# Performance work log

Hardware: AMD Instinct MI355X
Metric: run time of the kernel (lower is better)

Reference implementation:

```python
import math
import jax, jax.numpy as jnp
import numpy as np

D_MODEL = 1024
N_HEADS = 16
HEAD_DIM = D_MODEL // N_HEADS
B, L = 1, 4096


def _slopes(n_heads):
    ratio = 2.0 ** (-8.0 / n_heads)
    return jnp.asarray([ratio ** (i + 1) for i in range(n_heads)], dtype=jnp.float32)


def setup_inputs() -> dict:
    key = jax.random.key(0)
    ks = jax.random.split(key, 5)
    scale = 1.0 / math.sqrt(D_MODEL)
    return {
        "x": jax.random.normal(ks[0], (B, L, D_MODEL), dtype=jnp.float32),
        "q_w": jax.random.normal(ks[1], (D_MODEL, D_MODEL), dtype=jnp.float32) * scale,
        "k_w": jax.random.normal(ks[2], (D_MODEL, D_MODEL), dtype=jnp.float32) * scale,
        "v_w": jax.random.normal(ks[3], (D_MODEL, D_MODEL), dtype=jnp.float32) * scale,
        "o_w": jax.random.normal(ks[4], (D_MODEL, D_MODEL), dtype=jnp.float32) * scale,
    }


def reference(x, q_w, k_w, v_w, o_w):
    b, l, _ = x.shape
    # projections -> [B, H, L, hd]
    def proj(w):
        return (x @ w).reshape(b, l, N_HEADS, HEAD_DIM).transpose(0, 2, 1, 3)
    q, k, v = proj(q_w), proj(k_w), proj(v_w)

    scale = math.sqrt(HEAD_DIM)
    scores = jnp.einsum("bhid,bhjd->bhij", q, k) / scale  # [B,H,L,L]

    pos = jnp.arange(l)
    distance = jnp.abs(pos[None, :] - pos[:, None]).astype(jnp.float32)  # [L,L]
    alibi = -distance[None, :, :] * _slopes(N_HEADS)[:, None, None]       # [H,L,L]
    scores = scores + alibi[None]

    causal = pos[None, :] <= pos[:, None]  # j <= i
    scores = jnp.where(causal[None, None], scores, -jnp.inf)

    attn = jax.nn.softmax(scores, axis=-1)
    out = jnp.einsum("bhij,bhjd->bhid", attn, v)
    out = out.transpose(0, 2, 1, 3).reshape(b, l, D_MODEL)
    return out @ o_w
```

## Files before the change

kernel.cpp:

```cpp
#include <hip/hip_runtime.h>

#define L_SEQ 4096
#define DM    1024
#define NH    16
#define HD    64

typedef unsigned short ushort_t;
typedef __attribute__((ext_vector_type(8))) short bf16x8;
typedef __attribute__((ext_vector_type(4))) float f32x4;

__device__ inline unsigned short f2bf(float f) {
    union { float f; unsigned int u; } v; v.f = f;
    unsigned int r = v.u + 0x7fffu + ((v.u >> 16) & 1u);
    return (unsigned short)(r >> 16);
}

__device__ inline unsigned cvt_pk_bf16(float lo, float hi) {
    unsigned w;
    asm("v_cvt_pk_bf16_f32 %0, %1, %2" : "=v"(w) : "v"(lo), "v"(hi));
    return w;
}

__device__ inline void load_lds16(const ushort_t* g, ushort_t* l) {
    __builtin_amdgcn_global_load_lds(
        (const __attribute__((address_space(1))) unsigned int*)g,
        (__attribute__((address_space(3))) unsigned int*)l, 16, 0, 0);
}

__device__ inline bool detect_f32(const ushort_t* xraw) {
    __shared__ int s_flag;
    const int t = threadIdx.x;
    if (t < 64) {
        unsigned e = (xraw[2 * t] >> 7) & 0xFFu;
        unsigned long long m = __ballot(e >= 0x88u);
        if (t == 0) s_flag = (__popcll(m) >= 8) ? 1 : 0;
    }
    __syncthreads();
    return s_flag != 0;
}

__global__ __launch_bounds__(256) void convert_all(const void* __restrict__ xv,
                                                   const void* __restrict__ w0,
                                                   const void* __restrict__ w1,
                                                   const void* __restrict__ w2,
                                                   const void* __restrict__ w3,
                                                   ushort_t* __restrict__ xb,
                                                   ushort_t* __restrict__ wT) {
    bool f32 = detect_f32((const ushort_t*)xv);
    const int z = blockIdx.z;
    const int t = threadIdx.x;

    if (z == 4) {
        const int B0 = (blockIdx.y * 16 + blockIdx.x) * 16384;
        #pragma unroll
        for (int it = 0; it < 8; ++it) {
            const int i = B0 + it * 2048 + t * 8;
            if (f32) {
                const float* xf = (const float*)xv;
                float4 v0 = *(const float4*)(xf + i);
                float4 v1 = *(const float4*)(xf + i + 4);
                uint4 u;
                u.x = cvt_pk_bf16(v0.x, v0.y);
                u.y = cvt_pk_bf16(v0.z, v0.w);
                u.z = cvt_pk_bf16(v1.x, v1.y);
                u.w = cvt_pk_bf16(v1.z, v1.w);
                *(uint4*)(xb + i) = u;
            } else {
                *(uint4*)(xb + i) = *(const uint4*)((const ushort_t*)xv + i);
            }
        }
        return;
    }

    const void* w = (z == 0) ? w0 : (z == 1) ? w1 : (z == 2) ? w2 : w3;
    ushort_t* out = wT + (size_t)z * (DM * DM);
    __shared__ ushort_t T[64][65];
    const int k0 = blockIdx.x * 64, n0 = blockIdx.y * 64;
    #pragma unroll
    for (int i = 0; i < 16; ++i) {
        int e = t + i * 256;
        int r = e >> 6, c = e & 63;
        T[r][c] = f32 ? f2bf(((const float*)w)[(size_t)(k0 + r) * DM + n0 + c])
                      : ((const ushort_t*)w)[(size_t)(k0 + r) * DM + n0 + c];
    }
    __syncthreads();
    #pragma unroll
    for (int i = 0; i < 16; ++i) {
        int e = t + i * 256;
        int d = e >> 6, l = e & 63;
        out[(size_t)(n0 + d) * DM + k0 + l] = T[l][d];
    }
}

__device__ inline void gemm128_body(const ushort_t* __restrict__ A,
                                    const ushort_t* __restrict__ Bt,
                                    void* __restrict__ Cv, int cmode,
                                    int m0, int n0) {
    constexpr int K = 1024, NOUT = 1024;
    __shared__ ushort_t As[128 * 64];
    __shared__ ushort_t Bs[128 * 64];

    const int t = threadIdx.x, lane = t & 63, wave = t >> 6;
    const int l15 = lane & 15, quad = lane >> 4;
    const int mw = (wave >> 1) * 64, nw = (wave & 1) * 64;
    const int srow = lane >> 3;
    const int sgr  = (lane & 7) ^ (lane >> 3);
    const int swz  = l15 & 7;

    f32x4 acc[4][4] = {};

    for (int k0 = 0; k0 < K; k0 += 64) {
        #pragma unroll
        for (int i = 0; i < 4; ++i) {
            const int j = wave * 4 + i;
            load_lds16(A  + (size_t)(m0 + 8 * j + srow) * K + k0 + sgr * 8,
                       &As[8 * j * 64]);
            load_lds16(Bt + (size_t)(n0 + 8 * j + srow) * K + k0 + sgr * 8,
                       &Bs[8 * j * 64]);
        }
        __syncthreads();

        #pragma unroll
        for (int kt = 0; kt < 2; ++kt) {
            bf16x8 af[4], bf[4];
            #pragma unroll
            for (int i = 0; i < 4; ++i) {
                af[i] = *(const bf16x8*)&As[(mw + i * 16 + l15) * 64
                                            + (((kt * 4 + quad) ^ swz) * 8)];
                bf[i] = *(const bf16x8*)&Bs[(nw + i * 16 + l15) * 64
                                            + (((kt * 4 + quad) ^ swz) * 8)];
            }
            #pragma unroll
            for (int mt = 0; mt < 4; ++mt)
                #pragma unroll
                for (int nt = 0; nt < 4; ++nt)
                    acc[mt][nt] = __builtin_amdgcn_mfma_f32_16x16x32_bf16(
                        af[mt], bf[nt], acc[mt][nt], 0, 0, 0);
        }
        __syncthreads();
    }

    if (cmode == 2) {
        ushort_t* Vt = (ushort_t*)Cv;
        #pragma unroll
        for (int mt = 0; mt < 4; ++mt)
            #pragma unroll
            for (int nt = 0; nt < 4; ++nt) {
                int col  = n0 + nw + nt * 16 + l15;
                int row0 = m0 + mw + mt * 16 + quad * 4;
                ushort_t pk[4] = {f2bf(acc[mt][nt][0]), f2bf(acc[mt][nt][1]),
                                  f2bf(acc[mt][nt][2]), f2bf(acc[mt][nt][3])};
                *(uint2*)&Vt[(size_t)col * L_SEQ + row0] = *(const uint2*)pk;
            }
        return;
    }

    const int odd = lane & 1;
    #pragma unroll
    for (int mtp = 0; mtp < 2; ++mtp)
        #pragma unroll
        for (int nt = 0; nt < 4; ++nt)
            #pragma unroll
            for (int r = 0; r < 4; ++r) {
                float zA = acc[2 * mtp][nt][r];
                float zB = acc[2 * mtp + 1][nt][r];
                float send = odd ? zA : zB;
                float got  = __shfl_xor(send, 1);
                const int row = m0 + mw + (2 * mtp + odd) * 16 + quad * 4 + r;
                const int col = n0 + nw + nt * 16 + (l15 & ~1);
                if (cmode == 1) {
                    float2 w2 = odd ? make_float2(got, zB) : make_float2(zA, got);
                    *(float2*)((float*)Cv + (size_t)row * NOUT + col) = w2;
                } else {
                    float lo = odd ? got : zA;
                    float hi = odd ? zB  : got;
                    unsigned w = cvt_pk_bf16(lo, hi);
                    *(unsigned*)((ushort_t*)Cv + (size_t)row * NOUT + col) = w;
                }
            }
}

__global__ __launch_bounds__(256) void qkv128(const ushort_t* __restrict__ xb,
                                              const ushort_t* __restrict__ wT,
                                              ushort_t* Qp, ushort_t* Kp, ushort_t* Vt) {
    const int b = blockIdx.x;
    const int n0 = (b & 7) * 128;
    const int u  = b >> 3;
    const int m0 = (u / 3) * 128;
    const int z  = u % 3;
    const ushort_t* Bt = wT + (size_t)z * (DM * DM);
    if (z == 0)      gemm128_body(xb, Bt, Qp, 0, m0, n0);
    else if (z == 1) gemm128_body(xb, Bt, Kp, 0, m0, n0);
    else             gemm128_body(xb, Bt, Vt, 2, m0, n0);
}

__global__ __launch_bounds__(256) void ogemm128(const void* __restrict__ xdet,
                                                const ushort_t* __restrict__ An,
                                                const ushort_t* __restrict__ woT,
                                                void* __restrict__ C) {
    bool f32 = detect_f32((const ushort_t*)xdet);
    const int b = blockIdx.x;
    const int n0 = (b & 7) * 128, m0 = (b >> 3) * 128;
    gemm128_body(An, woT, C, f32 ? 1 : 0, m0, n0);
}

__global__ __launch_bounds__(256) void attn_kernel(const ushort_t* __restrict__ Q,
                                                   const ushort_t* __restrict__ Kp,
                                                   const ushort_t* __restrict__ Vt,
                                                   ushort_t* __restrict__ O) {
    __shared__ ushort_t Ks[2][128 * 64];
    __shared__ ushort_t Vs[2][64 * 128];
    __shared__ ushort_t Pt[64 * 128];

    const int b    = blockIdx.x;
    const int h    = 2 * (b & 7) + ((b >> 3) & 1);
    const int bx   = b >> 4;
    const int t    = threadIdx.x;
    const int lane = t & 63, wave = t >> 6;
    const int l15  = lane & 15, quad = lane >> 4;
    const float LOG2E  = 1.44269504f;
    const float slope2 = exp2f(-0.5f * (float)(h + 1)) * LOG2E;
    const float c0     = 0.125f * LOG2E;
    const float qd4f   = (float)(quad * 4);

    const int krow = lane >> 3, kgr = (lane & 7) ^ (lane >> 3);
    const int vsub = lane >> 4;
    const int swz = l15 & 7;

    auto stage_load = [&](int buf, int kv0) {
        #pragma unroll
        for (int i = 0; i < 4; ++i) {
            const int j = wave * 4 + i;
            const int r = 8 * j + krow;
            load_lds16(Kp + (size_t)(kv0 + r) * DM + h * HD + kgr * 8,
                       &Ks[buf][8 * j * 64]);
        }
        #pragma unroll
        for (int i = 0; i < 4; ++i) {
            const int j = wave * 4 + i;
            const int d = 4 * j + vsub;
            const int g = (lane & 15) ^ (4 * (j & 1) + vsub);
            load_lds16(Vt + (size_t)(h * HD + d) * L_SEQ + kv0 + g * 8,
                       &Vs[buf][4 * j * 128]);
        }
    };

    int par = 0;
    stage_load(0, 0);

    #pragma unroll
    for (int half = 0; half < 2; ++half) {
        const int qb = half ? bx : (63 - bx);
        const int q0 = qb * 64;
        const int qg = q0 + wave * 16 + l15;
        const float qf = (float)qg;

        bf16x8 bq[2];
        #pragma unroll
        for (int kt = 0; kt < 2; ++kt)
            bq[kt] = *(const bf16x8*)(Q + (size_t)qg * DM + h * HD + kt * 32 + quad * 8);

        f32x4 acc_o[4] = {};
        float l_r = 0.f;

        const int nst = (qb + 2) >> 1;
        for (int s = 0; s < nst; ++s) {
            const int kv0 = s * 128;
            __syncthreads();

            const int nkv0 = (s + 1 < nst) ? (s + 1) * 128 : 0;
            stage_load(par ^ 1, nkv0);

            f32x4 sacc[8];
            #pragma unroll
            for (int mt = 0; mt < 8; ++mt) sacc[mt] = (f32x4){0.f, 0.f, 0.f, 0.f};
            #pragma unroll
            for (int kt = 0; kt < 2; ++kt)
                #pragma unroll
                for (int mt = 0; mt < 8; ++mt) {
                    bf16x8 a = *(const bf16x8*)&Ks[par][(mt * 16 + l15) * 64
                                                        + (((kt * 4 + quad) ^ swz) * 8)];
                    sacc[mt] = __builtin_amdgcn_mfma_f32_16x16x32_bf16(a, bq[kt], sacc[mt], 0, 0, 0);
                }

            const bool diag = (kv0 + 128 > q0);
            const float off = slope2 * ((float)kv0 + qd4f - qf);
            float rs = 0.f;
            #pragma unroll
            for (int mt = 0; mt < 8; ++mt)
                #pragma unroll
                for (int r = 0; r < 4; ++r) {
                    float kvl = (float)(mt * 16 + r);
                    float s2  = fmaf(sacc[mt][r], c0, fmaf(slope2, kvl, off));
                    if (diag) {
                        int kvg = kv0 + mt * 16 + quad * 4 + r;
                        s2 = (kvg <= qg) ? s2 : -1e30f;
                    }
                    float p = exp2f(s2);
                    sacc[mt][r] = p;
                    rs += p;
                }
            rs += __shfl_xor(rs, 16);
            rs += __shfl_xor(rs, 32);
            l_r += rs;

            #pragma unroll
            for (int mt = 0; mt < 8; ++mt) {
                union { float f; unsigned u; } a0, a1, a2, a3;
                a0.f = sacc[mt][0]; a1.f = sacc[mt][1];
                a2.f = sacc[mt][2]; a3.f = sacc[mt][3];
                uint2 w;
                w.x = __builtin_amdgcn_perm(a1.u, a0.u, 0x07060302);
                w.y = __builtin_amdgcn_perm(a3.u, a2.u, 0x07060302);
                const int g = mt * 2 + (quad >> 1);
                *(uint2*)&Pt[(wave * 16 + l15) * 128
                             + ((g ^ swz) * 8 + (quad & 1) * 4)] = w;
            }
            __threadfence_block();

            #pragma unroll
            for (int kt = 0; kt < 4; ++kt) {
                bf16x8 a = *(const bf16x8*)&Pt[(wave * 16 + l15) * 128
                                               + (((kt * 4 + quad) ^ swz) * 8)];
                #pragma unroll
                for (int nt = 0; nt < 4; ++nt) {
                    bf16x8 bvv = *(const bf16x8*)&Vs[par][(nt * 16 + l15) * 128
                                                          + (((kt * 4 + quad) ^ swz) * 8)];
                    acc_o[nt] = __builtin_amdgcn_mfma_f32_16x16x32_bf16(a, bvv, acc_o[nt], 0, 0, 0);
                }
            }

            par ^= 1;
        }

        float linv[4];
        #pragma unroll
        for (int r = 0; r < 4; ++r) linv[r] = 1.0f / __shfl(l_r, quad * 4 + r);
        #pragma unroll
        for (int nt = 0; nt < 4; ++nt)
            #pragma unroll
            for (int r = 0; r < 4; ++r) {
                int row = q0 + wave * 16 + quad * 4 + r;
                O[(size_t)row * DM + h * HD + nt * 16 + l15] = f2bf(acc_o[nt][r] * linv[r]);
            }
    }
}

extern "C" void kernel_launch(void* const* d_in, const int* in_sizes, int n_in,
                              void* d_out, int out_size, void* d_ws, size_t ws_size,
                              hipStream_t stream) {
    const void* x  = d_in[0];
    const void* wq = d_in[1];
    const void* wk = d_in[2];
    const void* wv = d_in[3];
    const void* wo = d_in[4];

    const size_t SZ = (size_t)L_SEQ * DM;
    const size_t WZ = (size_t)DM * DM;
    ushort_t* xb = (ushort_t*)d_ws;
    ushort_t* wT = xb + SZ;
    ushort_t* Qp = wT + 4 * WZ;
    ushort_t* Kp = Qp + SZ;
    ushort_t* Vt = Kp + SZ;
    ushort_t* An = xb;

    convert_all<<<dim3(16, 16, 5), 256, 0, stream>>>(x, wq, wk, wv, wo, xb, wT);
    qkv128<<<768, 256, 0, stream>>>(xb, wT, Qp, Kp, Vt);
    attn_kernel<<<512, 256, 0, stream>>>(Qp, Kp, Vt, An);
    ogemm128<<<256, 256, 0, stream>>>(x, An, wT + 3 * WZ, d_out);
}
```

Measured before the change: 243.7 us.

## Fuse paired causal query blocks into one KV sweep sharing K/V tiles

Each attention block previously processed its two paired query blocks (63-bx and bx) in sequence, loading every K/V tile twice for the overlapping prefix. Now both query blocks run in a single loop over KV tiles. Each staged K/V tile is reused for block B while B is still in range. Block index order is also remapped so pairings alternate in workload across the grid. This roughly halves K/V LDS staging traffic and barriers for the short block. The cost is more registers for the two accumulator sets and score arrays, which may lower occupancy.

```diff
diff --git a/kernel.cpp b/kernel.cpp
--- a/kernel.cpp
+++ b/kernel.cpp
@@ -214,7 +214,8 @@
 
     const int b    = blockIdx.x;
     const int h    = 2 * (b & 7) + ((b >> 3) & 1);
-    const int bx   = b >> 4;
+    const int pi   = b >> 4;
+    const int bx   = (pi < 16) ? pi : (47 - pi);
     const int t    = threadIdx.x;
     const int lane = t & 63, wave = t >> 6;
     const int l15  = lane & 15, quad = lane >> 4;
@@ -245,70 +246,135 @@
         }
     };
 
+    const int qbA = 63 - bx, qbB = bx;
+    const int q0A = qbA * 64, q0B = qbB * 64;
+    const int qgA = q0A + wave * 16 + l15;
+    const int qgB = q0B + wave * 16 + l15;
+    const float qfA = (float)qgA, qfB = (float)qgB;
+    const int nstA = (qbA + 2) >> 1;
+    const int nstB = (qbB + 2) >> 1;
+
+    bf16x8 bqA[2], bqB[2];
+    #pragma unroll
+    for (int kt = 0; kt < 2; ++kt) {
+        bqA[kt] = *(const bf16x8*)(Q + (size_t)qgA * DM + h * HD + kt * 32 + quad * 8);
+        bqB[kt] = *(const bf16x8*)(Q + (size_t)qgB * DM + h * HD + kt * 32 + quad * 8);
+    }
+
+    f32x4 accA[4] = {}, accB[4] = {};
+    float lA = 0.f, lB = 0.f;
+
     int par = 0;
     stage_load(0, 0);
 
-    #pragma unroll
-    for (int half = 0; half < 2; ++half) {
-        const int qb = half ? bx : (63 - bx);
-        const int q0 = qb * 64;
-        const int qg = q0 + wave * 16 + l15;
-        const float qf = (float)qg;
-
-        bf16x8 bq[2];
+    for (int s = 0; s < nstA; ++s) {
+        const int kv0 = s * 128;
+        const bool doB = (s < nstB);
+        __syncthreads();
+
+        const int nkv0 = (s + 1 < nstA) ? (s + 1) * 128 : 0;
+        stage_load(par ^ 1, nkv0);
+
+        f32x4 sA[8], sB[8];
+        #pragma unroll
+        for (int mt = 0; mt < 8; ++mt) sA[mt] = (f32x4){0.f, 0.f, 0.f, 0.f};
         #pragma unroll
         for (int kt = 0; kt < 2; ++kt)
-            bq[kt] = *(const bf16x8*)(Q + (size_t)qg * DM + h * HD + kt * 32 + quad * 8);
-
-        f32x4 acc_o[4] = {};
-        float l_r = 0.f;
-
-        const int nst = (qb + 2) >> 1;
-        for (int s = 0; s < nst; ++s) {
-            const int kv0 = s * 128;
-            __syncthreads();
-
-            const int nkv0 = (s + 1 < nst) ? (s + 1) * 128 : 0;
-            stage_load(par ^ 1, nkv0);
-
-            f32x4 sacc[8];
-            #pragma unroll
-            for (int mt = 0; mt < 8; ++mt) sacc[mt] = (f32x4){0.f, 0.f, 0.f, 0.f};
+            #pragma unroll
+            for (int mt = 0; mt < 8; ++mt) {
+                bf16x8 a = *(const bf16x8*)&Ks[par][(mt * 16 + l15) * 64
+                                                    + (((kt * 4 + quad) ^ swz) * 8)];
+                sA[mt] = __builtin_amdgcn_mfma_f32_16x16x32_bf16(a, bqA[kt], sA[mt], 0, 0, 0);
+            }
+        if (doB) {
+            #pragma unroll
+            for (int mt = 0; mt < 8; ++mt) sB[mt] = (f32x4){0.f, 0.f, 0.f, 0.f};
             #pragma unroll
             for (int kt = 0; kt < 2; ++kt)
                 #pragma unroll
                 for (int mt = 0; mt < 8; ++mt) {
                     bf16x8 a = *(const bf16x8*)&Ks[par][(mt * 16 + l15) * 64
                                                         + (((kt * 4 + quad) ^ swz) * 8)];
-                    sacc[mt] = __builtin_amdgcn_mfma_f32_16x16x32_bf16(a, bq[kt], sacc[mt], 0, 0, 0);
+                    sB[mt] = __builtin_amdgcn_mfma_f32_16x16x32_bf16(a, bqB[kt], sB[mt], 0, 0, 0);
                 }
-
-            const bool diag = (kv0 + 128 > q0);
-            const float off = slope2 * ((float)kv0 + qd4f - qf);
+        }
+
+        {
+            const bool diag = (kv0 + 128 > q0A);
+            const float off = slope2 * ((float)kv0 + qd4f - qfA);
             float rs = 0.f;
             #pragma unroll
             for (int mt = 0; mt < 8; ++mt)
                 #pragma unroll
                 for (int r = 0; r < 4; ++r) {
                     float kvl = (float)(mt * 16 + r);
-                    float s2  = fmaf(sacc[mt][r], c0, fmaf(slope2, kvl, off));
+                    float s2  = fmaf(sA[mt][r], c0, fmaf(slope2, kvl, off));
                     if (diag) {
                         int kvg = kv0 + mt * 16 + quad * 4 + r;
-                        s2 = (kvg <= qg) ? s2 : -1e30f;
+                        s2 = (kvg <= qgA) ? s2 : -1e30f;
                     }
                     float p = exp2f(s2);
-                    sacc[mt][r] = p;
+                    sA[mt][r] = p;
                     rs += p;
                 }
             rs += __shfl_xor(rs, 16);
             rs += __shfl_xor(rs, 32);
-            l_r += rs;
-
+            lA += rs;
+        }
+
+        #pragma unroll
+        for (int mt = 0; mt < 8; ++mt) {
+            union { float f; unsigned u; } a0, a1, a2, a3;
+            a0.f = sA[mt][0]; a1.f = sA[mt][1];
+            a2.f = sA[mt][2]; a3.f = sA[mt][3];
+            uint2 w;
+            w.x = __builtin_amdgcn_perm(a1.u, a0.u, 0x07060302);
+            w.y = __builtin_amdgcn_perm(a3.u, a2.u, 0x07060302);
+            const int g = mt * 2 + (quad >> 1);
+            *(uint2*)&Pt[(wave * 16 + l15) * 128
+                         + ((g ^ swz) * 8 + (quad & 1) * 4)] = w;
+        }
+        __threadfence_block();
+        #pragma unroll
+        for (int kt = 0; kt < 4; ++kt) {
+            bf16x8 a = *(const bf16x8*)&Pt[(wave * 16 + l15) * 128
+                                           + (((kt * 4 + quad) ^ swz) * 8)];
+            #pragma unroll
+            for (int nt = 0; nt < 4; ++nt) {
+                bf16x8 bvv = *(const bf16x8*)&Vs[par][(nt * 16 + l15) * 128
+                                                      + (((kt * 4 + quad) ^ swz) * 8)];
+                accA[nt] = __builtin_amdgcn_mfma_f32_16x16x32_bf16(a, bvv, accA[nt], 0, 0, 0);
+            }
+        }
+
+        if (doB) {
+            const bool diag = (kv0 + 128 > q0B);
+            const float off = slope2 * ((float)kv0 + qd4f - qfB);
+            float rs = 0.f;
+            #pragma unroll
+            for (int mt = 0; mt < 8; ++mt)
+                #pragma unroll
+                for (int r = 0; r < 4; ++r) {
+                    float kvl = (float)(mt * 16 + r);
+                    float s2  = fmaf(sB[mt][r], c0, fmaf(slope2, kvl, off));
+                    if (diag) {
+                        int kvg = kv0 + mt * 16 + quad * 4 + r;
+                        s2 = (kvg <= qgB) ? s2 : -1e30f;
+                    }
+                    float p = exp2f(s2);
+                    sB[mt][r] = p;
+                    rs += p;
+                }
+            rs += __shfl_xor(rs, 16);
+            rs += __shfl_xor(rs, 32);
+            lB += rs;
+
+            __threadfence_block();
             #pragma unroll
             for (int mt = 0; mt < 8; ++mt) {
                 union { float f; unsigned u; } a0, a1, a2, a3;
-                a0.f = sacc[mt][0]; a1.f = sacc[mt][1];
-                a2.f = sacc[mt][2]; a3.f = sacc[mt][3];
+                a0.f = sB[mt][0]; a1.f = sB[mt][1];
+                a2.f = sB[mt][2]; a3.f = sB[mt][3];
                 uint2 w;
                 w.x = __builtin_amdgcn_perm(a1.u, a0.u, 0x07060302);
                 w.y = __builtin_amdgcn_perm(a3.u, a2.u, 0x07060302);
@@ -317,7 +383,6 @@
                              + ((g ^ swz) * 8 + (quad & 1) * 4)] = w;
             }
             __threadfence_block();
-
             #pragma unroll
             for (int kt = 0; kt < 4; ++kt) {
                 bf16x8 a = *(const bf16x8*)&Pt[(wave * 16 + l15) * 128
@@ -326,22 +391,36 @@
                 for (int nt = 0; nt < 4; ++nt) {
                     bf16x8 bvv = *(const bf16x8*)&Vs[par][(nt * 16 + l15) * 128
                                                           + (((kt * 4 + quad) ^ swz) * 8)];
-                    acc_o[nt] = __builtin_amdgcn_mfma_f32_16x16x32_bf16(a, bvv, acc_o[nt], 0, 0, 0);
+                    accB[nt] = __builtin_amdgcn_mfma_f32_16x16x32_bf16(a, bvv, accB[nt], 0, 0, 0);
                 }
             }
-
-            par ^= 1;
-        }
-
+        }
+
+        par ^= 1;
+    }
+
+    {
         float linv[4];
         #pragma unroll
-        for (int r = 0; r < 4; ++r) linv[r] = 1.0f / __shfl(l_r, quad * 4 + r);
+        for (int r = 0; r < 4; ++r) linv[r] = 1.0f / __shfl(lA, quad * 4 + r);
         #pragma unroll
         for (int nt = 0; nt < 4; ++nt)
             #pragma unroll
             for (int r = 0; r < 4; ++r) {
-                int row = q0 + wave * 16 + quad * 4 + r;
-                O[(size_t)row * DM + h * HD + nt * 16 + l15] = f2bf(acc_o[nt][r] * linv[r]);
+                int row = q0A + wave * 16 + quad * 4 + r;
+                O[(size_t)row * DM + h * HD + nt * 16 + l15] = f2bf(accA[nt][r] * linv[r]);
+            }
+    }
+    {
+        float linv[4];
+        #pragma unroll
+        for (int r = 0; r < 4; ++r) linv[r] = 1.0f / __shfl(lB, quad * 4 + r);
+        #pragma unroll
+        for (int nt = 0; nt < 4; ++nt)
+            #pragma unroll
+            for (int r = 0; r < 4; ++r) {
+                int row = q0B + wave * 16 + quad * 4 + r;
+                O[(size_t)row * DM + h * HD + nt * 16 + l15] = f2bf(accB[nt][r] * linv[r]);
             }
     }
 }
```

After: 293.2 us. 1.2x slower.
